# Performance work log

Measured on AMD Instinct MI355X. Metric: run time of the kernel, lower is better.

## Reference

```python
import jax, jax.numpy as jnp
import numpy as np

SHARED = 128  # matches TabularLoss(shared=128)


def _pairwise_dist(x, y):
    """Batched pairwise L2 distances. x: (B,N,D), y: (B,M,D) -> (B,N,M)."""
    sq = (jnp.sum(x * x, axis=-1)[:, :, None]
          + jnp.sum(y * y, axis=-1)[:, None, :]
          - 2.0 * jnp.einsum('bnd,bmd->bnm', x, y))
    sq = jnp.maximum(sq, 0.0)
    # safe sqrt (exact forward, no NaN grads at 0)
    return jnp.where(sq > 0, jnp.sqrt(jnp.where(sq > 0, sq, 1.0)), 0.0)


def _energy_distance(x, y):
    """geomloss SamplesLoss(loss='energy') with uniform weights.
    L = <a, D_xy b> - 0.5 <a, D_xx a> - 0.5 <b, D_yy b>, a=b=1/N.
    Returns per-batch losses, shape (B,)."""
    dxy = jnp.mean(_pairwise_dist(x, y), axis=(-2, -1))
    dxx = jnp.mean(_pairwise_dist(x, x), axis=(-2, -1))
    dyy = jnp.mean(_pairwise_dist(y, y), axis=(-2, -1))
    return dxy - 0.5 * dxx - 0.5 * dyy


def setup_inputs() -> dict:
    key = jax.random.key(0)
    k1, k2 = jax.random.split(key)
    total, genes = 8192, 5000
    return {
        'input': jax.random.normal(k1, (total, genes), dtype=jnp.float32),
        'target': jax.random.normal(k2, (total, genes), dtype=jnp.float32),
        'downsample': 64,
    }


def reference(input, target, downsample):
    x = input.reshape(-1, downsample, input.shape[-1])   # (B, N, G)
    y = target.reshape(-1, downsample, target.shape[-1])
    # gene-level MMD: each cell group is a point cloud of N cells in G dims
    gene_mmd = jnp.nanmean(_energy_distance(x, y))
    # cell-level MMD: transpose(2,0) -> (S, N, B): per shared gene, N points in B dims
    cx = jnp.transpose(x[:, :, -SHARED:], (2, 1, 0))
    cy = jnp.transpose(y[:, :, -SHARED:], (2, 1, 0))
    cell_mmd = jnp.nanmean(_energy_distance(cx, cy))
    loss = (jnp.where(jnp.isnan(gene_mmd), 0.0, gene_mmd)
            + jnp.where(jnp.isnan(cell_mmd), 0.0, cell_mmd))
    return loss
```

## Files before the change

kernel.cpp:

```cpp
#include <hip/hip_runtime.h>
#include <math.h>

#define TOTAL   8192
#define GENES   5000
#define NDS     64
#define NB      128
#define NSHARED 128
#define KC      64

#define GRAM_OFF 64

typedef __attribute__((ext_vector_type(8)))  short        short8;
typedef __attribute__((ext_vector_type(4)))  unsigned int uint4v;
typedef __attribute__((ext_vector_type(16))) float        f32x16;

typedef const __attribute__((address_space(1))) void* GPTR;
typedef __attribute__((address_space(3))) void*       LPTR;

#define GLOAD16(gp, lp) \
    __builtin_amdgcn_global_load_lds((GPTR)(gp), (LPTR)(lp), 16, 0, 0)

static __device__ inline unsigned int hpack2(float f0, float f1) {
    const unsigned int u0 = __builtin_bit_cast(unsigned int, f0) + 0x8000u;
    const unsigned int u1 = __builtin_bit_cast(unsigned int, f1) + 0x8000u;
    return (u1 & 0xFFFF0000u) | (u0 >> 16);
}
static __device__ inline short8 ldcvt_h(const float* base, int sw, int c0) {
    const float4 a = *(const float4*)(base + (((c0    ) ^ sw) << 2));
    const float4 b = *(const float4*)(base + (((c0 + 1) ^ sw) << 2));
    uint4v hv;
    hv[0] = hpack2(a.x, a.y); hv[1] = hpack2(a.z, a.w);
    hv[2] = hpack2(b.x, b.y); hv[3] = hpack2(b.z, b.w);
    return __builtin_bit_cast(short8, hv);
}

__global__ __launch_bounds__(256, 2)
void k_main(const float* __restrict__ X, const float* __restrict__ Y,
            const float* __restrict__ zsrc, float* __restrict__ grams,
            float* __restrict__ acc, int splitD, int Dper) {
    __shared__ __align__(16) float smem[16384];
    const int t = threadIdx.x;

    if ((int)blockIdx.x >= NSHARED) {
        const int blk = blockIdx.x - NSHARED;
        const int b = blk / splitD, c = blk % splitD;
        const int d0 = c * Dper;
        const int d1 = min(GENES, d0 + Dper);

        const float* __restrict__ xb = X + (size_t)b * NDS * GENES;
        const float* __restrict__ yb = Y + (size_t)b * NDS * GENES;

        float* sX = smem;
        float* sY = smem + 2 * NDS * KC;

        const int lane = t & 63;
        const int w    = t >> 6;
        const int qr   = w >> 1, qc = w & 1;
        const int lm   = lane & 31;
        const int kh2  = (lane >> 5) << 1;

        const int mr  = (qr << 5) + lm;
        const int mc  = (qc << 5) + lm;
        const int swr = mr & 15, swc = mc & 15;

        const int s16  = lane & 15;
        const int rsub = lane >> 4;
        const int rA = (w << 4) + rsub;
        const int rB = rA + 4, rC = rA + 8, rD = rA + 12;
        const int cA = (s16 ^ (rA & 15)) << 2;
        const int cB = (s16 ^ (rB & 15)) << 2;
        const int cC = (s16 ^ (rC & 15)) << 2;
        const int cD = (s16 ^ (rD & 15)) << 2;
        const float* gxA = xb + (size_t)rA * GENES + cA;
        const float* gxB = xb + (size_t)rB * GENES + cB;
        const float* gxC = xb + (size_t)rC * GENES + cC;
        const float* gxD = xb + (size_t)rD * GENES + cD;
        const float* gyA = yb + (size_t)rA * GENES + cA;
        const float* gyB = yb + (size_t)rB * GENES + cB;
        const float* gyC = yb + (size_t)rC * GENES + cC;
        const float* gyD = yb + (size_t)rD * GENES + cD;
        const int lA = ((w << 4) + 0) * KC;
        const int lB = lA + 4 * KC, lC = lA + 8 * KC, lD = lA + 12 * KC;

#define STAGEBUF(bofs, dd) do {                                               \
    const float* pxA = ((dd) + cA + 4 <= d1) ? gxA + (dd) : zsrc;             \
    const float* pxB = ((dd) + cB + 4 <= d1) ? gxB + (dd) : zsrc;             \
    const float* pxC = ((dd) + cC + 4 <= d1) ? gxC + (dd) : zsrc;             \
    const float* pxD = ((dd) + cD + 4 <= d1) ? gxD + (dd) : zsrc;             \
    const float* pyA = ((dd) + cA + 4 <= d1) ? gyA + (dd) : zsrc;             \
    const float* pyB = ((dd) + cB + 4 <= d1) ? gyB + (dd) : zsrc;             \
    const float* pyC = ((dd) + cC + 4 <= d1) ? gyC + (dd) : zsrc;             \
    const float* pyD = ((dd) + cD + 4 <= d1) ? gyD + (dd) : zsrc;             \
    GLOAD16(pxA, sX + (bofs) + lA);                                           \
    GLOAD16(pxB, sX + (bofs) + lB);                                           \
    GLOAD16(pxC, sX + (bofs) + lC);                                           \
    GLOAD16(pxD, sX + (bofs) + lD);                                           \
    GLOAD16(pyA, sY + (bofs) + lA);                                           \
    GLOAD16(pyB, sY + (bofs) + lB);                                           \
    GLOAD16(pyC, sY + (bofs) + lC);                                           \
    GLOAD16(pyD, sY + (bofs) + lD);                                           \
} while (0)

        f32x16 axy = {0,0,0,0,0,0,0,0,0,0,0,0,0,0,0,0};
        f32x16 axx = {0,0,0,0,0,0,0,0,0,0,0,0,0,0,0,0};
        f32x16 ayy = {0,0,0,0,0,0,0,0,0,0,0,0,0,0,0,0};

        const int nchunks = (d1 - d0 + KC - 1) / KC;

        STAGEBUF(0, d0);
        __syncthreads();

        for (int ci = 0; ci < nchunks; ++ci) {
            const int bofs = (ci & 1) * (NDS * KC);
            if (ci + 1 < nchunks)
                STAGEBUF(((ci + 1) & 1) * (NDS * KC), d0 + (ci + 1) * KC);

            const float* xrow = sX + bofs + mr * KC;
            const float* yrow = sY + bofs + mr * KC;
            const float* xcol = sX + bofs + mc * KC;
            const float* ycol = sY + bofs + mc * KC;
#pragma unroll
            for (int ks = 0; ks < 4; ++ks) {
                const int c0 = (ks << 2) + kh2;
                const short8 xr = ldcvt_h(xrow, swr, c0);
                const short8 yr = ldcvt_h(yrow, swr, c0);
                const short8 xc = ldcvt_h(xcol, swc, c0);
                const short8 yc = ldcvt_h(ycol, swc, c0);
                axy = __builtin_amdgcn_mfma_f32_32x32x16_bf16(xr, yc, axy, 0, 0, 0);
                axx = __builtin_amdgcn_mfma_f32_32x32x16_bf16(xr, xc, axx, 0, 0, 0);
                ayy = __builtin_amdgcn_mfma_f32_32x32x16_bf16(yr, yc, ayy, 0, 0, 0);
            }
            __syncthreads();
        }
#undef STAGEBUF

        float* g = grams + (size_t)(b * splitD + c) * 3 * 4096;
        const int col = (qc << 5) + lm;
#pragma unroll
        for (int r = 0; r < 16; ++r) {
            const int row = (qr << 5) + (r & 3) + ((r >> 2) << 3) + ((lane >> 5) << 2);
            g[0 * 4096 + row * 64 + col] = axy[r];
            g[1 * 4096 + row * 64 + col] = axx[r];
            g[2 * 4096 + row * 64 + col] = ayy[r];
        }
        return;
    }

    {
        const int s   = blockIdx.x;
        const int col = GENES - NSHARED + s;
        float* lds = smem;

#pragma unroll
        for (int k = 0; k < 32; ++k) {
            const int idx = t + 256 * k;
            lds[idx]        = X[(size_t)idx * GENES + col];
            lds[8192 + idx] = Y[(size_t)idx * GENES + col];
        }
        __syncthreads();

        const int ti = t & 15, tj = t >> 4;
        const int i0 = ti << 2, j0 = tj << 2;
        float axy[4][4] = {{0}}, axx[4][4] = {{0}}, ayy[4][4] = {{0}};

#pragma unroll 4
        for (int bb = 0; bb < NB; ++bb) {
            const float4 xi4 = *(const float4*)(lds + bb * 64 + i0);
            const float4 xj4 = *(const float4*)(lds + bb * 64 + j0);
            const float4 yi4 = *(const float4*)(lds + 8192 + bb * 64 + i0);
            const float4 yj4 = *(const float4*)(lds + 8192 + bb * 64 + j0);
            const float* xi = &xi4.x;
            const float* xj = &xj4.x;
            const float* yi = &yi4.x;
            const float* yj = &yj4.x;
#pragma unroll
            for (int ii = 0; ii < 4; ++ii) {
#pragma unroll
                for (int jj = 0; jj < 4; ++jj) {
                    axy[ii][jj] = fmaf(xi[ii], yj[jj], axy[ii][jj]);
                    axx[ii][jj] = fmaf(xi[ii], xj[jj], axx[ii][jj]);
                    ayy[ii][jj] = fmaf(yi[ii], yj[jj], ayy[ii][jj]);
                }
            }
        }
        __syncthreads();
#pragma unroll
        for (int ii = 0; ii < 4; ++ii) {
            float4 v;
            v.x = axy[ii][0]; v.y = axy[ii][1]; v.z = axy[ii][2]; v.w = axy[ii][3];
            *(float4*)(lds + 0 * 4096 + (i0 + ii) * 64 + j0) = v;
            v.x = axx[ii][0]; v.y = axx[ii][1]; v.z = axx[ii][2]; v.w = axx[ii][3];
            *(float4*)(lds + 1 * 4096 + (i0 + ii) * 64 + j0) = v;
            v.x = ayy[ii][0]; v.y = ayy[ii][1]; v.z = ayy[ii][2]; v.w = ayy[ii][3];
            *(float4*)(lds + 2 * 4096 + (i0 + ii) * 64 + j0) = v;
        }
        __syncthreads();

        float local = 0.f;
#pragma unroll
        for (int k = 0; k < 16; ++k) {
            const int e = t + 256 * k;
            const int i = e >> 6, j = e & 63;
            const float gxy = lds[e];
            const float gxx = lds[4096 + e];
            const float gyy = lds[8192 + e];
            const float nxi = lds[4096 + i * 65], nxj = lds[4096 + j * 65];
            const float nyi = lds[8192 + i * 65], nyj = lds[8192 + j * 65];
            const float dxy = sqrtf(fmaxf(nxi + nyj - 2.f * gxy, 0.f));
            const float dxx = sqrtf(fmaxf(nxi + nxj - 2.f * gxx, 0.f));
            const float dyy = sqrtf(fmaxf(nyi + nyj - 2.f * gyy, 0.f));
            local += dxy - 0.5f * (dxx + dyy);
        }
#pragma unroll
        for (int off = 32; off; off >>= 1) local += __shfl_down(local, off);
        __syncthreads();
        if ((t & 63) == 0) lds[t >> 6] = local;
        __syncthreads();
        if (t == 0) {
            const float bl = lds[0] + lds[1] + lds[2] + lds[3];
            atomicAdd(acc + 1, bl * (1.0f / (4096.0f * (float)NSHARED)));
        }
    }
}

__global__ __launch_bounds__(256) void k_gene_dist(const float* __restrict__ grams,
                                                   float* __restrict__ acc,
                                                   int* __restrict__ done,
                                                   float* __restrict__ out,
                                                   int splitD) {
    const int b = blockIdx.x, t = threadIdx.x;
    __shared__ __align__(16) float G[3 * 4096];
    __shared__ float red[4];

    for (int m = 0; m < 3; ++m) {
#pragma unroll
        for (int k = 0; k < 16; ++k) {
            const int e = t + 256 * k;
            float s = 0.f;
            for (int c = 0; c < splitD; ++c)
                s += grams[((size_t)(b * splitD + c) * 3 + m) * 4096 + e];
            G[m * 4096 + e] = s;
        }
    }
    __syncthreads();

    float local = 0.f;
#pragma unroll
    for (int k = 0; k < 16; ++k) {
        const int e = t + 256 * k;
        const int i = e >> 6, j = e & 63;
        const float gxy = G[e];
        const float gxx = G[4096 + e];
        const float gyy = G[8192 + e];
        const float nxi = G[4096 + i * 65], nxj = G[4096 + j * 65];
        const float nyi = G[8192 + i * 65], nyj = G[8192 + j * 65];
        const float dxy = sqrtf(fmaxf(nxi + nyj - 2.f * gxy, 0.f));
        const float dxx = sqrtf(fmaxf(nxi + nxj - 2.f * gxx, 0.f));
        const float dyy = sqrtf(fmaxf(nyi + nyj - 2.f * gyy, 0.f));
        local += dxy - 0.5f * (dxx + dyy);
    }
#pragma unroll
    for (int off = 32; off; off >>= 1) local += __shfl_down(local, off);
    if ((t & 63) == 0) red[t >> 6] = local;
    __syncthreads();
    if (t == 0) {
        const float bl = red[0] + red[1] + red[2] + red[3];
        atomicAdd(acc, bl * (1.0f / (4096.0f * (float)NB)));
        __threadfence();
        const int old = __hip_atomic_fetch_add(done, 1, __ATOMIC_ACQ_REL,
                                               __HIP_MEMORY_SCOPE_AGENT);
        if (old == NB - 1) {
            const float a0 = __hip_atomic_load(acc, __ATOMIC_RELAXED,
                                               __HIP_MEMORY_SCOPE_AGENT);
            const float a1 = __hip_atomic_load(acc + 1, __ATOMIC_RELAXED,
                                               __HIP_MEMORY_SCOPE_AGENT);
            out[0] = a0 + a1;
        }
    }
}

extern "C" void kernel_launch(void* const* d_in, const int* in_sizes, int n_in,
                              void* d_out, int out_size, void* d_ws, size_t ws_size,
                              hipStream_t stream) {
    const float* X = (const float*)d_in[0];
    const float* Y = (const float*)d_in[1];
    float* out = (float*)d_out;
    float* ws  = (float*)d_ws;

    int splitD = 4;
    while (splitD > 1 &&
           ((size_t)GRAM_OFF + (size_t)splitD * NB * 3 * 4096) * sizeof(float) > ws_size)
        splitD >>= 1;
    const int chunks = (GENES + KC - 1) / KC;
    const int cper   = (chunks + splitD - 1) / splitD;
    const int Dper   = cper * KC;

    float* acc   = ws;
    float* zsrc  = ws + 32;
    int*   done  = (int*)(ws + 48);
    float* grams = ws + GRAM_OFF;

    hipMemsetAsync(ws, 0, GRAM_OFF * sizeof(float), stream);
    hipLaunchKernelGGL(k_main, dim3(NSHARED + NB * splitD), dim3(256), 0, stream,
                       X, Y, zsrc, grams, acc, splitD, Dper);
    hipLaunchKernelGGL(k_gene_dist, dim3(NB), dim3(256), 0, stream,
                       grams, acc, done, out, splitD);
}
```

Before: 161.1 us.

## Pre-convert gene slices to bf16 in workspace before MFMA staging

Each gram block first converts its fp32 input slice to bf16 and writes it to a padded workspace buffer. It then streams the bf16 copy into LDS with async global-to-LDS loads, so the inner loop no longer unpacks fp32 values. The goal is to halve the LDS footprint per chunk and drop the per-iteration conversion work. The cost is an extra global write and re-read of the slice, which may be served from L2. The fp32 path is kept as a fallback when workspace is too small.

```diff
diff --git a/kernel.cpp b/kernel.cpp
--- a/kernel.cpp
+++ b/kernel.cpp
@@ -7,6 +7,7 @@
 #define NB      128
 #define NSHARED 128
 #define KC      64
+#define GP      5120
 
 #define GRAM_OFF 64
 
@@ -34,53 +35,248 @@
     return __builtin_bit_cast(short8, hv);
 }
 
+static __device__ inline void cell_path(const float* __restrict__ X,
+                                        const float* __restrict__ Y,
+                                        float* __restrict__ acc,
+                                        float* lds, int t) {
+    const int s   = blockIdx.x;
+    const int col = GENES - NSHARED + s;
+#pragma unroll
+    for (int k = 0; k < 32; ++k) {
+        const int idx = t + 256 * k;
+        lds[idx]        = X[(size_t)idx * GENES + col];
+        lds[8192 + idx] = Y[(size_t)idx * GENES + col];
+    }
+    __syncthreads();
+    const int ti = t & 15, tj = t >> 4;
+    const int i0 = ti << 2, j0 = tj << 2;
+    float axy[4][4] = {{0}}, axx[4][4] = {{0}}, ayy[4][4] = {{0}};
+#pragma unroll 4
+    for (int bb = 0; bb < NB; ++bb) {
+        const float4 xi4 = *(const float4*)(lds + bb * 64 + i0);
+        const float4 xj4 = *(const float4*)(lds + bb * 64 + j0);
+        const float4 yi4 = *(const float4*)(lds + 8192 + bb * 64 + i0);
+        const float4 yj4 = *(const float4*)(lds + 8192 + bb * 64 + j0);
+        const float* xi = &xi4.x;
+        const float* xj = &xj4.x;
+        const float* yi = &yi4.x;
+        const float* yj = &yj4.x;
+#pragma unroll
+        for (int ii = 0; ii < 4; ++ii)
+#pragma unroll
+            for (int jj = 0; jj < 4; ++jj) {
+                axy[ii][jj] = fmaf(xi[ii], yj[jj], axy[ii][jj]);
+                axx[ii][jj] = fmaf(xi[ii], xj[jj], axx[ii][jj]);
+                ayy[ii][jj] = fmaf(yi[ii], yj[jj], ayy[ii][jj]);
+            }
+    }
+    __syncthreads();
+#pragma unroll
+    for (int ii = 0; ii < 4; ++ii) {
+        float4 v;
+        v.x = axy[ii][0]; v.y = axy[ii][1]; v.z = axy[ii][2]; v.w = axy[ii][3];
+        *(float4*)(lds + 0 * 4096 + (i0 + ii) * 64 + j0) = v;
+        v.x = axx[ii][0]; v.y = axx[ii][1]; v.z = axx[ii][2]; v.w = axx[ii][3];
+        *(float4*)(lds + 1 * 4096 + (i0 + ii) * 64 + j0) = v;
+        v.x = ayy[ii][0]; v.y = ayy[ii][1]; v.z = ayy[ii][2]; v.w = ayy[ii][3];
+        *(float4*)(lds + 2 * 4096 + (i0 + ii) * 64 + j0) = v;
+    }
+    __syncthreads();
+    float local = 0.f;
+#pragma unroll
+    for (int k = 0; k < 16; ++k) {
+        const int e = t + 256 * k;
+        const int i = e >> 6, j = e & 63;
+        const float gxy = lds[e];
+        const float gxx = lds[4096 + e];
+        const float gyy = lds[8192 + e];
+        const float nxi = lds[4096 + i * 65], nxj = lds[4096 + j * 65];
+        const float nyi = lds[8192 + i * 65], nyj = lds[8192 + j * 65];
+        const float dxy = sqrtf(fmaxf(nxi + nyj - 2.f * gxy, 0.f));
+        const float dxx = sqrtf(fmaxf(nxi + nxj - 2.f * gxx, 0.f));
+        const float dyy = sqrtf(fmaxf(nyi + nyj - 2.f * gyy, 0.f));
+        local += dxy - 0.5f * (dxx + dyy);
+    }
+#pragma unroll
+    for (int off = 32; off; off >>= 1) local += __shfl_down(local, off);
+    __syncthreads();
+    if ((t & 63) == 0) lds[t >> 6] = local;
+    __syncthreads();
+    if (t == 0) {
+        const float bl = lds[0] + lds[1] + lds[2] + lds[3];
+        atomicAdd(acc + 1, bl * (1.0f / (4096.0f * (float)NSHARED)));
+    }
+}
+
+static __device__ inline void gram_writeout(float* g, int qr, int qc, int lane,
+                                            const f32x16 axy, const f32x16 axx,
+                                            const f32x16 ayy) {
+    const int col = (qc << 5) + (lane & 31);
+#pragma unroll
+    for (int r = 0; r < 16; ++r) {
+        const int row = (qr << 5) + (r & 3) + ((r >> 2) << 3) + ((lane >> 5) << 2);
+        g[0 * 4096 + row * 64 + col] = axy[r];
+        g[1 * 4096 + row * 64 + col] = axx[r];
+        g[2 * 4096 + row * 64 + col] = ayy[r];
+    }
+}
+
 __global__ __launch_bounds__(256, 2)
-void k_main(const float* __restrict__ X, const float* __restrict__ Y,
-            const float* __restrict__ zsrc, float* __restrict__ grams,
-            float* __restrict__ acc, int splitD, int Dper) {
+void k_main_bf16(const float* __restrict__ X, const float* __restrict__ Y,
+                 unsigned short* __restrict__ bfX,
+                 unsigned short* __restrict__ bfY,
+                 float* __restrict__ grams, float* __restrict__ acc,
+                 int splitD, int Dper) {
     __shared__ __align__(16) float smem[16384];
     const int t = threadIdx.x;
 
-    if ((int)blockIdx.x >= NSHARED) {
-        const int blk = blockIdx.x - NSHARED;
-        const int b = blk / splitD, c = blk % splitD;
-        const int d0 = c * Dper;
-        const int d1 = min(GENES, d0 + Dper);
-
-        const float* __restrict__ xb = X + (size_t)b * NDS * GENES;
-        const float* __restrict__ yb = Y + (size_t)b * NDS * GENES;
-
-        float* sX = smem;
-        float* sY = smem + 2 * NDS * KC;
-
-        const int lane = t & 63;
-        const int w    = t >> 6;
-        const int qr   = w >> 1, qc = w & 1;
-        const int lm   = lane & 31;
-        const int kh2  = (lane >> 5) << 1;
-
-        const int mr  = (qr << 5) + lm;
-        const int mc  = (qc << 5) + lm;
-        const int swr = mr & 15, swc = mc & 15;
-
-        const int s16  = lane & 15;
-        const int rsub = lane >> 4;
-        const int rA = (w << 4) + rsub;
-        const int rB = rA + 4, rC = rA + 8, rD = rA + 12;
-        const int cA = (s16 ^ (rA & 15)) << 2;
-        const int cB = (s16 ^ (rB & 15)) << 2;
-        const int cC = (s16 ^ (rC & 15)) << 2;
-        const int cD = (s16 ^ (rD & 15)) << 2;
-        const float* gxA = xb + (size_t)rA * GENES + cA;
-        const float* gxB = xb + (size_t)rB * GENES + cB;
-        const float* gxC = xb + (size_t)rC * GENES + cC;
-        const float* gxD = xb + (size_t)rD * GENES + cD;
-        const float* gyA = yb + (size_t)rA * GENES + cA;
-        const float* gyB = yb + (size_t)rB * GENES + cB;
-        const float* gyC = yb + (size_t)rC * GENES + cC;
-        const float* gyD = yb + (size_t)rD * GENES + cD;
-        const int lA = ((w << 4) + 0) * KC;
-        const int lB = lA + 4 * KC, lC = lA + 8 * KC, lD = lA + 12 * KC;
+    if ((int)blockIdx.x < NSHARED) { cell_path(X, Y, acc, smem, t); return; }
+
+    const int blk = blockIdx.x - NSHARED;
+    const int b = blk / splitD, c = blk % splitD;
+    const int d0 = c * Dper;
+    const int d1 = min(GENES, d0 + Dper);
+
+    const int lane = t & 63;
+    const int w    = t >> 6;
+    const int qr   = w >> 1, qc = w & 1;
+    const int lm   = lane & 31;
+    const int kh   = lane >> 5;
+
+    const int mr = (qr << 5) + lm;
+    const int mc = (qc << 5) + lm;
+
+    {
+        const float* xb = X + (size_t)b * NDS * GENES;
+        const float* yb = Y + (size_t)b * NDS * GENES;
+        unsigned short* bxb = bfX + (size_t)b * NDS * GP;
+        unsigned short* byb = bfY + (size_t)b * NDS * GP;
+        for (int rr = 0; rr < 16; ++rr) {
+            const int row = (w << 4) + rr;
+            const float* sx = xb + (size_t)row * GENES;
+            const float* sy = yb + (size_t)row * GENES;
+            unsigned short* dx = bxb + (size_t)row * GP;
+            unsigned short* dy = byb + (size_t)row * GP;
+#pragma unroll
+            for (int j = 0; j < 5; ++j) {
+                const int col = d0 + ((lane + (j << 6)) << 2);
+                float4 vx = {0.f, 0.f, 0.f, 0.f};
+                float4 vy = {0.f, 0.f, 0.f, 0.f};
+                if (col + 4 <= GENES) {
+                    vx = *(const float4*)(sx + col);
+                    vy = *(const float4*)(sy + col);
+                }
+                uint2 ux, uy;
+                ux.x = hpack2(vx.x, vx.y); ux.y = hpack2(vx.z, vx.w);
+                uy.x = hpack2(vy.x, vy.y); uy.y = hpack2(vy.z, vy.w);
+                *(uint2*)(dx + col) = ux;
+                *(uint2*)(dy + col) = uy;
+            }
+        }
+    }
+    __syncthreads();
+
+    unsigned short* sXb = (unsigned short*)smem;
+    unsigned short* sYb = (unsigned short*)smem + 8192;
+
+    const int srow = lane >> 3;
+    const int gblk = (lane & 7) ^ srow;
+    const int rowA = (w << 4) + srow;
+    const unsigned short* gxA = bfX + ((size_t)b * NDS + rowA) * GP + gblk * 8;
+    const unsigned short* gyA = bfY + ((size_t)b * NDS + rowA) * GP + gblk * 8;
+    const unsigned short* gxB = gxA + 8 * GP;
+    const unsigned short* gyB = gyA + 8 * GP;
+    const int lA = w << 10;
+
+#define STAGEBUF(bofs, dd) do {                          \
+    GLOAD16(gxA + (dd), sXb + (bofs) + lA);              \
+    GLOAD16(gxB + (dd), sXb + (bofs) + lA + 512);        \
+    GLOAD16(gyA + (dd), sYb + (bofs) + lA);              \
+    GLOAD16(gyB + (dd), sYb + (bofs) + lA + 512);        \
+} while (0)
+
+    f32x16 axy = {0,0,0,0,0,0,0,0,0,0,0,0,0,0,0,0};
+    f32x16 axx = {0,0,0,0,0,0,0,0,0,0,0,0,0,0,0,0};
+    f32x16 ayy = {0,0,0,0,0,0,0,0,0,0,0,0,0,0,0,0};
+
+    const int nchunks = (d1 - d0 + KC - 1) / KC;
+
+    STAGEBUF(0, d0);
+    __syncthreads();
+
+    for (int ci = 0; ci < nchunks; ++ci) {
+        const int bofs = (ci & 1) << 12;
+        if (ci + 1 < nchunks)
+            STAGEBUF(((ci + 1) & 1) << 12, d0 + (ci + 1) * KC);
+#pragma unroll
+        for (int ks = 0; ks < 4; ++ks) {
+            const int ls = (ks << 1) + kh;
+            const int er = bofs + (mr << 6) + ((ls ^ (mr & 7)) << 3);
+            const int ec = bofs + (mc << 6) + ((ls ^ (mc & 7)) << 3);
+            const short8 xr = *(const short8*)&sXb[er];
+            const short8 yr = *(const short8*)&sYb[er];
+            const short8 xc = *(const short8*)&sXb[ec];
+            const short8 yc = *(const short8*)&sYb[ec];
+            axy = __builtin_amdgcn_mfma_f32_32x32x16_bf16(xr, yc, axy, 0, 0, 0);
+            axx = __builtin_amdgcn_mfma_f32_32x32x16_bf16(xr, xc, axx, 0, 0, 0);
+            ayy = __builtin_amdgcn_mfma_f32_32x32x16_bf16(yr, yc, ayy, 0, 0, 0);
+        }
+        __syncthreads();
+    }
+#undef STAGEBUF
+
+    gram_writeout(grams + (size_t)(b * splitD + c) * 3 * 4096,
+                  qr, qc, lane, axy, axx, ayy);
+}
+
+__global__ __launch_bounds__(256, 2)
+void k_main_f32(const float* __restrict__ X, const float* __restrict__ Y,
+                const float* __restrict__ zsrc, float* __restrict__ grams,
+                float* __restrict__ acc, int splitD, int Dper) {
+    __shared__ __align__(16) float smem[16384];
+    const int t = threadIdx.x;
+
+    if ((int)blockIdx.x < NSHARED) { cell_path(X, Y, acc, smem, t); return; }
+
+    const int blk = blockIdx.x - NSHARED;
+    const int b = blk / splitD, c = blk % splitD;
+    const int d0 = c * Dper;
+    const int d1 = min(GENES, d0 + Dper);
+
+    const float* __restrict__ xb = X + (size_t)b * NDS * GENES;
+    const float* __restrict__ yb = Y + (size_t)b * NDS * GENES;
+
+    float* sX = smem;
+    float* sY = smem + 2 * NDS * KC;
+
+    const int lane = t & 63;
+    const int w    = t >> 6;
+    const int qr   = w >> 1, qc = w & 1;
+    const int lm   = lane & 31;
+    const int kh2  = (lane >> 5) << 1;
+
+    const int mr  = (qr << 5) + lm;
+    const int mc  = (qc << 5) + lm;
+    const int swr = mr & 15, swc = mc & 15;
+
+    const int s16  = lane & 15;
+    const int rsub = lane >> 4;
+    const int rA = (w << 4) + rsub;
+    const int rB = rA + 4, rC = rA + 8, rD = rA + 12;
+    const int cA = (s16 ^ (rA & 15)) << 2;
+    const int cB = (s16 ^ (rB & 15)) << 2;
+    const int cC = (s16 ^ (rC & 15)) << 2;
+    const int cD = (s16 ^ (rD & 15)) << 2;
+    const float* gxA = xb + (size_t)rA * GENES + cA;
+    const float* gxB = xb + (size_t)rB * GENES + cB;
+    const float* gxC = xb + (size_t)rC * GENES + cC;
+    const float* gxD = xb + (size_t)rD * GENES + cD;
+    const float* gyA = yb + (size_t)rA * GENES + cA;
+    const float* gyB = yb + (size_t)rB * GENES + cB;
+    const float* gyC = yb + (size_t)rC * GENES + cC;
+    const float* gyD = yb + (size_t)rD * GENES + cD;
+    const int lA = ((w << 4) + 0) * KC;
+    const int lB = lA + 4 * KC, lC = lA + 8 * KC, lD = lA + 12 * KC;
 
 #define STAGEBUF(bofs, dd) do {                                               \
     const float* pxA = ((dd) + cA + 4 <= d1) ? gxA + (dd) : zsrc;             \
@@ -101,126 +297,41 @@
     GLOAD16(pyD, sY + (bofs) + lD);                                           \
 } while (0)
 
-        f32x16 axy = {0,0,0,0,0,0,0,0,0,0,0,0,0,0,0,0};
-        f32x16 axx = {0,0,0,0,0,0,0,0,0,0,0,0,0,0,0,0};
-        f32x16 ayy = {0,0,0,0,0,0,0,0,0,0,0,0,0,0,0,0};
-
-        const int nchunks = (d1 - d0 + KC - 1) / KC;
-
-        STAGEBUF(0, d0);
-        __syncthreads();
-
-        for (int ci = 0; ci < nchunks; ++ci) {
-            const int bofs = (ci & 1) * (NDS * KC);
-            if (ci + 1 < nchunks)
-                STAGEBUF(((ci + 1) & 1) * (NDS * KC), d0 + (ci + 1) * KC);
-
-            const float* xrow = sX + bofs + mr * KC;
-            const float* yrow = sY + bofs + mr * KC;
-            const float* xcol = sX + bofs + mc * KC;
-            const float* ycol = sY + bofs + mc * KC;
-#pragma unroll
-            for (int ks = 0; ks < 4; ++ks) {
-                const int c0 = (ks << 2) + kh2;
-                const short8 xr = ldcvt_h(xrow, swr, c0);
-                const short8 yr = ldcvt_h(yrow, swr, c0);
-                const short8 xc = ldcvt_h(xcol, swc, c0);
-                const short8 yc = ldcvt_h(ycol, swc, c0);
-                axy = __builtin_amdgcn_mfma_f32_32x32x16_bf16(xr, yc, axy, 0, 0, 0);
-                axx = __builtin_amdgcn_mfma_f32_32x32x16_bf16(xr, xc, axx, 0, 0, 0);
-                ayy = __builtin_amdgcn_mfma_f32_32x32x16_bf16(yr, yc, ayy, 0, 0, 0);
-            }
-            __syncthreads();
-        }
-#undef STAGEBUF
-
-        float* g = grams + (size_t)(b * splitD + c) * 3 * 4096;
-        const int col = (qc << 5) + lm;
-#pragma unroll
-        for (int r = 0; r < 16; ++r) {
-            const int row = (qr << 5) + (r & 3) + ((r >> 2) << 3) + ((lane >> 5) << 2);
-            g[0 * 4096 + row * 64 + col] = axy[r];
-            g[1 * 4096 + row * 64 + col] = axx[r];
-            g[2 * 4096 + row * 64 + col] = ayy[r];
-        }
-        return;
-    }
-
-    {
-        const int s   = blockIdx.x;
-        const int col = GENES - NSHARED + s;
-        float* lds = smem;
-
-#pragma unroll
-        for (int k = 0; k < 32; ++k) {
-            const int idx = t + 256 * k;
-            lds[idx]        = X[(size_t)idx * GENES + col];
-            lds[8192 + idx] = Y[(size_t)idx * GENES + col];
+    f32x16 axy = {0,0,0,0,0,0,0,0,0,0,0,0,0,0,0,0};
+    f32x16 axx = {0,0,0,0,0,0,0,0,0,0,0,0,0,0,0,0};
+    f32x16 ayy = {0,0,0,0,0,0,0,0,0,0,0,0,0,0,0,0};
+
+    const int nchunks = (d1 - d0 + KC - 1) / KC;
+
+    STAGEBUF(0, d0);
+    __syncthreads();
+
+    for (int ci = 0; ci < nchunks; ++ci) {
+        const int bofs = (ci & 1) * (NDS * KC);
+        if (ci + 1 < nchunks)
+            STAGEBUF(((ci + 1) & 1) * (NDS * KC), d0 + (ci + 1) * KC);
+
+        const float* xrow = sX + bofs + mr * KC;
+        const float* yrow = sY + bofs + mr * KC;
+        const float* xcol = sX + bofs + mc * KC;
+        const float* ycol = sY + bofs + mc * KC;
+#pragma unroll
+        for (int ks = 0; ks < 4; ++ks) {
+            const int c0 = (ks << 2) + kh2;
+            const short8 xr = ldcvt_h(xrow, swr, c0);
+            const short8 yr = ldcvt_h(yrow, swr, c0);
+            const short8 xc = ldcvt_h(xcol, swc, c0);
+            const short8 yc = ldcvt_h(ycol, swc, c0);
+            axy = __builtin_amdgcn_mfma_f32_32x32x16_bf16(xr, yc, axy, 0, 0, 0);
+            axx = __builtin_amdgcn_mfma_f32_32x32x16_bf16(xr, xc, axx, 0, 0, 0);
+            ayy = __builtin_amdgcn_mfma_f32_32x32x16_bf16(yr, yc, ayy, 0, 0, 0);
         }
         __syncthreads();
-
-        const int ti = t & 15, tj = t >> 4;
-        const int i0 = ti << 2, j0 = tj << 2;
-        float axy[4][4] = {{0}}, axx[4][4] = {{0}}, ayy[4][4] = {{0}};
-
-#pragma unroll 4
-        for (int bb = 0; bb < NB; ++bb) {
-            const float4 xi4 = *(const float4*)(lds + bb * 64 + i0);
-            const float4 xj4 = *(const float4*)(lds + bb * 64 + j0);
-            const float4 yi4 = *(const float4*)(lds + 8192 + bb * 64 + i0);
-            const float4 yj4 = *(const float4*)(lds + 8192 + bb * 64 + j0);
-            const float* xi = &xi4.x;
-            const float* xj = &xj4.x;
-            const float* yi = &yi4.x;
-            const float* yj = &yj4.x;
-#pragma unroll
-            for (int ii = 0; ii < 4; ++ii) {
-#pragma unroll
-                for (int jj = 0; jj < 4; ++jj) {
-                    axy[ii][jj] = fmaf(xi[ii], yj[jj], axy[ii][jj]);
-                    axx[ii][jj] = fmaf(xi[ii], xj[jj], axx[ii][jj]);
-                    ayy[ii][jj] = fmaf(yi[ii], yj[jj], ayy[ii][jj]);
-                }
-            }
-        }
-        __syncthreads();
-#pragma unroll
-        for (int ii = 0; ii < 4; ++ii) {
-            float4 v;
-            v.x = axy[ii][0]; v.y = axy[ii][1]; v.z = axy[ii][2]; v.w = axy[ii][3];
-            *(float4*)(lds + 0 * 4096 + (i0 + ii) * 64 + j0) = v;
-            v.x = axx[ii][0]; v.y = axx[ii][1]; v.z = axx[ii][2]; v.w = axx[ii][3];
-            *(float4*)(lds + 1 * 4096 + (i0 + ii) * 64 + j0) = v;
-            v.x = ayy[ii][0]; v.y = ayy[ii][1]; v.z = ayy[ii][2]; v.w = ayy[ii][3];
-            *(float4*)(lds + 2 * 4096 + (i0 + ii) * 64 + j0) = v;
-        }
-        __syncthreads();
-
-        float local = 0.f;
-#pragma unroll
-        for (int k = 0; k < 16; ++k) {
-            const int e = t + 256 * k;
-            const int i = e >> 6, j = e & 63;
-            const float gxy = lds[e];
-            const float gxx = lds[4096 + e];
-            const float gyy = lds[8192 + e];
-            const float nxi = lds[4096 + i * 65], nxj = lds[4096 + j * 65];
-            const float nyi = lds[8192 + i * 65], nyj = lds[8192 + j * 65];
-            const float dxy = sqrtf(fmaxf(nxi + nyj - 2.f * gxy, 0.f));
-            const float dxx = sqrtf(fmaxf(nxi + nxj - 2.f * gxx, 0.f));
-            const float dyy = sqrtf(fmaxf(nyi + nyj - 2.f * gyy, 0.f));
-            local += dxy - 0.5f * (dxx + dyy);
-        }
-#pragma unroll
-        for (int off = 32; off; off >>= 1) local += __shfl_down(local, off);
-        __syncthreads();
-        if ((t & 63) == 0) lds[t >> 6] = local;
-        __syncthreads();
-        if (t == 0) {
-            const float bl = lds[0] + lds[1] + lds[2] + lds[3];
-            atomicAdd(acc + 1, bl * (1.0f / (4096.0f * (float)NSHARED)));
-        }
-    }
+    }
+#undef STAGEBUF
+
+    gram_writeout(grams + (size_t)(b * splitD + c) * 3 * 4096,
+                  qr, qc, lane, axy, axx, ayy);
 }
 
 __global__ __launch_bounds__(256) void k_gene_dist(const float* __restrict__ grams,
@@ -300,9 +411,22 @@
     int*   done  = (int*)(ws + 48);
     float* grams = ws + GRAM_OFF;
 
+    const size_t gramFloats = (size_t)GRAM_OFF + (size_t)splitD * NB * 3 * 4096;
+    const size_t bfCount    = (size_t)TOTAL * GP;
+    const size_t needNew    = gramFloats * sizeof(float)
+                            + 2 * bfCount * sizeof(unsigned short);
+
     hipMemsetAsync(ws, 0, GRAM_OFF * sizeof(float), stream);
-    hipLaunchKernelGGL(k_main, dim3(NSHARED + NB * splitD), dim3(256), 0, stream,
-                       X, Y, zsrc, grams, acc, splitD, Dper);
+
+    if (splitD == 4 && Dper == 1280 && ws_size >= needNew) {
+        unsigned short* bfX = (unsigned short*)(ws + gramFloats);
+        unsigned short* bfY = bfX + bfCount;
+        hipLaunchKernelGGL(k_main_bf16, dim3(NSHARED + NB * splitD), dim3(256),
+                           0, stream, X, Y, bfX, bfY, grams, acc, splitD, Dper);
+    } else {
+        hipLaunchKernelGGL(k_main_f32, dim3(NSHARED + NB * splitD), dim3(256),
+                           0, stream, X, Y, zsrc, grams, acc, splitD, Dper);
+    }
     hipLaunchKernelGGL(k_gene_dist, dim3(NB), dim3(256), 0, stream,
                        grams, acc, done, out, splitD);
 }
```

Measured after the change: 232.2 us. 1.44x slower.
